# Kernel tuning notes

Hardware: AMD Instinct MI355X
Metric: run time of the kernel (lower is better)

## Reference

```python
import jax, jax.numpy as jnp
import numpy as np

B, N, T, F = 256, 64, 50, 2
E, H, R = 64, 128, 30


def setup_inputs() -> dict:
    key = jax.random.key(0)
    ks = jax.random.split(key, 16)
    rn = lambda k, shp, s=0.1: jax.random.normal(k, shp, jnp.float32) * s
    return {
        "src": jax.random.normal(ks[0], (B, N, T, F), jnp.float32),
        "trg": jax.random.normal(ks[1], (B, R, F), jnp.float32),
        # spatial encoder: residual Linear (no bias) + GCNConv weight/bias
        "W_res": rn(ks[2], (F, E)),
        "W_gcn": rn(ks[3], (F, E)),
        "b_gcn": jnp.zeros((E,), jnp.float32),
        # encoder LSTMCell (PyTorch gate order i,f,g,o); b = b_ih + b_hh fused
        "W_ih_e": rn(ks[4], (E, 4 * H)),
        "W_hh_e": rn(ks[5], (H, 4 * H)),
        "b_e": jnp.zeros((4 * H,), jnp.float32),
        # decoder: linear1 (2->E), LSTMCell (E->H), linear2 (H->2)
        "W1": rn(ks[6], (F, E)),
        "b1": jnp.zeros((E,), jnp.float32),
        "W_ih_d": rn(ks[7], (E, 4 * H)),
        "W_hh_d": rn(ks[8], (H, 4 * H)),
        "b_d": jnp.zeros((4 * H,), jnp.float32),
        "W2": rn(ks[9], (H, F)),
        "b2": jnp.zeros((F,), jnp.float32),
    }


def _lstm_step(h, c, xt, W_ih, W_hh, b):
    g = xt @ W_ih + h @ W_hh + b
    i, f, gg, o = jnp.split(g, 4, axis=-1)
    c = jax.nn.sigmoid(f) * c + jax.nn.sigmoid(i) * jnp.tanh(gg)
    h = jax.nn.sigmoid(o) * jnp.tanh(c)
    return h, c


def _forward(src, trg, W_res, W_gcn, b_gcn, W_ih_e, W_hh_e, b_e,
             W1, b1, W_ih_d, W_hh_d, b_d, W2, b2):
    # ---- EncoderSpatial: distance-weighted GCNConv over per-(sample,t) full graph ----
    x = jnp.swapaxes(src, 1, 2)                       # [B,T,N,F]
    diff = x[:, :, :, None, :] - x[:, :, None, :, :]  # [B,T,N,N,F]
    dist = jnp.linalg.norm(diff, axis=-1)             # [B,T,N,N]
    dist = jnp.where(dist == 0.0, 1e-6, dist)
    w = jnp.minimum(1.0 / dist, 1.0)                  # clipped inverse distance
    eye = jnp.eye(N, dtype=x.dtype)
    w = w * (1.0 - eye) + eye                         # remove self loops, GCN adds them with weight 1
    dinv = jnp.sum(w, axis=-1) ** -0.5                # [B,T,N]
    A = w * dinv[..., :, None] * dinv[..., None, :]   # sym-normalized adjacency
    gcn = jnp.einsum('btij,btjf->btif', A, x @ W_gcn) + b_gcn
    enc = jax.nn.relu(gcn + x @ W_res)                # [B,T,N,E]
    emb = enc[:, :, 0, :]                             # target-agent embeddings [B,T,E]
    inputs0 = x[:, :, 0, :]                           # target-agent positions  [B,T,F]

    # ---- LSTM encoder over T steps ----
    def enc_step(carry, xt):
        h, c = _lstm_step(carry[0], carry[1], xt, W_ih_e, W_hh_e, b_e)
        return (h, c), None
    h0 = jnp.zeros((B, H), src.dtype)
    (h, c), _ = jax.lax.scan(enc_step, (h0, h0), jnp.swapaxes(emb, 0, 1))

    def dec_step(carry, _):
        xin, h, c = carry
        ed = jax.nn.relu(xin @ W1 + b1)
        h, c = _lstm_step(h, c, ed, W_ih_d, W_hh_d, b_d)
        out = h @ W2 + b2
        return (out, h, c), out
    (_, _, _), outs = jax.lax.scan(dec_step, (inputs0[:, -1, :], h, c), None, length=R)
    return jnp.swapaxes(outs, 0, 1)                   # reg: [B,R,F]


def reference(src, trg, W_res, W_gcn, b_gcn, W_ih_e, W_hh_e, b_e,
              W1, b1, W_ih_d, W_hh_d, b_d, W2, b2):
    return _forward(src, trg, W_res, W_gcn, b_gcn, W_ih_e, W_hh_e, b_e,
                    W1, b1, W_ih_d, W_hh_d, b_d, W2, b2)
```

## Files before the change

### kernel.cpp

```cpp
#include <hip/hip_runtime.h>

#define Bn 256
#define Nn 64
#define Tn 50
#define Fn 2
#define En 64
#define Hn 128
#define Rn 30
#define G4 512

typedef _Float16 h2    __attribute__((ext_vector_type(2)));
typedef _Float16 f16x8 __attribute__((ext_vector_type(8)));
typedef float    f32x4 __attribute__((ext_vector_type(4)));

__device__ __forceinline__ float sigf(float x) {
    return __builtin_amdgcn_rcpf(1.0f + __expf(-x));
}
__device__ __forceinline__ float tanh_fast(float x) {
    return 1.0f - 2.0f * __builtin_amdgcn_rcpf(__expf(2.0f * x) + 1.0f);
}
__device__ __forceinline__ float dot2(h2 a, h2 b, float c) {
#if __has_builtin(__builtin_amdgcn_fdot2)
    return __builtin_amdgcn_fdot2(a, b, c, false);
#else
    return fmaf((float)a[0], (float)b[0], fmaf((float)a[1], (float)b[1], c));
#endif
}
__device__ __forceinline__ h2 pack2(float a, float b) {
    h2 r; r[0] = (_Float16)a; r[1] = (_Float16)b; return r;
}
__device__ __forceinline__ h2 bch2(float u)        { return __builtin_bit_cast(h2, u); }
__device__ __forceinline__ h2 bchu(unsigned int u) { return __builtin_bit_cast(h2, u); }

__device__ __forceinline__ void blockbar() {
    __builtin_amdgcn_sched_barrier(0);
    asm volatile("s_waitcnt lgkmcnt(0)" ::: "memory");
    __builtin_amdgcn_s_barrier();
    __builtin_amdgcn_sched_barrier(0);
}

__global__ __launch_bounds__(512) void k_pre(const float* __restrict__ src,
                                             const float* __restrict__ W_res,
                                             const float* __restrict__ W_gcn,
                                             const float* __restrict__ b_gcn,
                                             const float* __restrict__ W_ih_e,
                                             const float* __restrict__ b_e,
                                             _Float16* __restrict__ XI)
{
    const int tid  = threadIdx.x;
    const int lane = tid & 63;
    const int wv   = tid >> 6;
    const int task0 = blockIdx.x * 64;

    __shared__ __align__(16) _Float16 elds[64][64];
    __shared__ float2 xs[8][Nn];

    const float wg0 = W_gcn[lane], wg1 = W_gcn[En + lane];
    const float wr0 = W_res[lane], wr1 = W_res[En + lane];
    const float bg  = b_gcn[lane];

    for (int it = 0; it < 8; it++) {
        const int task = task0 + (wv << 3) + it;
        const int b = task / Tn;
        const int t = task - b * Tn;

        const float2 xv = *reinterpret_cast<const float2*>(
            src + (((size_t)b * Nn + lane) * Tn + t) * Fn);
        const float x0 = xv.x, x1 = xv.y;
        xs[wv][lane] = xv;

        float rowsum = 0.0f, w0 = 0.0f;
        #pragma unroll
        for (int k = 0; k < Nn; k++) {
            const float2 o = xs[wv][k];
            const float dx = x0 - o.x, dy = x1 - o.y;
            const float w = fminf(__builtin_amdgcn_rsqf(dx * dx + dy * dy), 1.0f);
            rowsum += w;
            if (k == 0) w0 = w;
        }
        const float dinv  = __builtin_amdgcn_rsqf(rowsum);
        const float dinv0 = __shfl(dinv, 0);
        const float a = w0 * dinv0 * dinv;

        float p0 = a * x0, p1 = a * x1;
        #pragma unroll
        for (int off = 32; off; off >>= 1) {
            p0 += __shfl_xor(p0, off);
            p1 += __shfl_xor(p1, off);
        }
        const float xa = __shfl(x0, 0);
        const float xb = __shfl(x1, 0);

        const float v = p0 * wg0 + p1 * wg1 + bg + xa * wr0 + xb * wr1;
        elds[(wv << 3) + it][lane] = (_Float16)fmaxf(v, 0.0f);
    }

    const int colp = (tid & 3) * 128 + (tid >> 2);
    h2 wih[32];
    #pragma unroll
    for (int q = 0; q < 32; q++)
        wih[q] = pack2(W_ih_e[(size_t)(2 * q) * G4 + colp],
                       W_ih_e[(size_t)(2 * q + 1) * G4 + colp]);
    const float be = b_e[colp];
    __syncthreads();

    for (int it = 0; it < 64; it++) {
        const float4* e4 = reinterpret_cast<const float4*>(&elds[it][0]);
        float acc = be;
        #pragma unroll
        for (int q = 0; q < 8; q++) {
            const float4 u = e4[q];
            acc = dot2(wih[4 * q + 0], bch2(u.x), acc);
            acc = dot2(wih[4 * q + 1], bch2(u.y), acc);
            acc = dot2(wih[4 * q + 2], bch2(u.z), acc);
            acc = dot2(wih[4 * q + 3], bch2(u.w), acc);
        }
        XI[(size_t)(task0 + it) * G4 + tid] = (_Float16)acc;
    }
}

__global__ __launch_bounds__(512) void k_seq(
    const _Float16* __restrict__ XI,
    const float* __restrict__ src,
    const float* __restrict__ W_hh_e,
    const float* __restrict__ W1,     const float* __restrict__ b1,
    const float* __restrict__ W_ih_d, const float* __restrict__ W_hh_d,
    const float* __restrict__ b_d,
    const float* __restrict__ W2,     const float* __restrict__ b2,
    float* __restrict__ out)
{
    const int tid  = threadIdx.x;
    const int lane = tid & 63;
    const int wv   = tid >> 6;
    const int l15  = lane & 15;
    const int lg   = lane >> 4;
    const int cc   = wv * 16 + l15;
    const int bq0  = blockIdx.x * 4;

    __shared__ __align__(16) _Float16 hbuf[2][576];
    __shared__ __align__(16) _Float16 edbuf[2][320];
    __shared__ __align__(16) _Float16 wi_frag[8 * 8 * 64 * 8];
    __shared__ __align__(16) float    redw[8][4][2];

    f16x8 bfr[4][4];
    #pragma unroll
    for (int g = 0; g < 4; g++)
        #pragma unroll
        for (int kt = 0; kt < 4; kt++) {
            f16x8 v;
            #pragma unroll
            for (int j = 0; j < 8; j++)
                v[j] = (_Float16)W_hh_e[(size_t)(kt * 32 + lg * 8 + j) * G4 + g * 128 + cc];
            bfr[g][kt] = v;
        }

    if (tid < 288) reinterpret_cast<float*>(&hbuf[0][0])[tid] = 0.0f;

    float cst = 0.0f;
    char* const hb0 = reinterpret_cast<char*>(&hbuf[0][0]);
    char* const hb1 = reinterpret_cast<char*>(&hbuf[1][0]);
    const _Float16* const XIrow = XI + (size_t)(bq0 + lg) * Tn * G4 + cc * 4;

    uint2 xi0, xi1;
    xi0 = *reinterpret_cast<const uint2*>(XIrow + 0 * G4);
    xi1 = *reinterpret_cast<const uint2*>(XIrow + 1 * G4);
    __syncthreads();

    for (int t = 0; t < Tn; t += 2) {
        uint2 nxt0, nxt1;
        const int t2 = (t + 2 < Tn) ? t + 2 : t;
        const int t3 = (t + 3 < Tn) ? t + 3 : t;
        nxt0 = *reinterpret_cast<const uint2*>(XIrow + (size_t)t2 * G4);
        nxt1 = *reinterpret_cast<const uint2*>(XIrow + (size_t)t3 * G4);

        #pragma unroll
        for (int half = 0; half < 2; half++) {
            char* const hr = half ? hb1 : hb0;
            char* const hw = half ? hb0 : hb1;
            const uint2 xiv = half ? xi1 : xi0;

            f16x8 af[4];
            #pragma unroll
            for (int kt = 0; kt < 4; kt++)
                af[kt] = *reinterpret_cast<const f16x8*>(
                    hr + (l15 & 3) * 288 + kt * 64 + lg * 16);

            f32x4 acc[4] = {};
            #pragma unroll
            for (int kt = 0; kt < 4; kt++)
                #pragma unroll
                for (int g = 0; g < 4; g++)
                    acc[g] = __builtin_amdgcn_mfma_f32_16x16x32_f16(af[kt], bfr[g][kt], acc[g], 0, 0, 0);

            float ga[4];
            #pragma unroll
            for (int g = 0; g < 4; g++) {
                const float s01 = (lg & 1) ? acc[g][1] : acc[g][0];
                const float s23 = (lg & 1) ? acc[g][3] : acc[g][2];
                ga[g] = (lg & 2) ? s23 : s01;
            }

            const h2 lo = bchu(xiv.x);
            const h2 hi = bchu(xiv.y);
            const float gi = ga[0] + (float)lo[0];
            const float gf = ga[1] + (float)lo[1];
            const float gg = ga[2] + (float)hi[0];
            const float go = ga[3] + (float)hi[1];
            cst = sigf(gf) * cst + sigf(gi) * tanh_fast(gg);
            const float hv = sigf(go) * tanh_fast(cst);

            *reinterpret_cast<_Float16*>(hw + lg * 288 + cc * 2) = (_Float16)hv;
            blockbar();
        }
        xi0 = nxt0; xi1 = nxt1;
    }

    #pragma unroll
    for (int g = 0; g < 4; g++)
        #pragma unroll
        for (int kt = 0; kt < 4; kt++) {
            f16x8 v;
            #pragma unroll
            for (int j = 0; j < 8; j++)
                v[j] = (_Float16)W_hh_d[(size_t)(kt * 32 + lg * 8 + j) * G4 + g * 128 + cc];
            bfr[g][kt] = v;
        }
    #pragma unroll
    for (int g = 0; g < 4; g++)
        #pragma unroll
        for (int kt2 = 0; kt2 < 2; kt2++) {
            f16x8 v;
            #pragma unroll
            for (int j = 0; j < 8; j++)
                v[j] = (_Float16)W_ih_d[(size_t)(kt2 * 32 + lg * 8 + j) * G4 + g * 128 + cc];
            *reinterpret_cast<f16x8*>(&wi_frag[((wv * 8 + g * 2 + kt2) * 64 + lane) * 8]) = v;
        }

    const float bd0 = b_d[cc], bd1 = b_d[128 + cc], bd2 = b_d[256 + cc], bd3 = b_d[384 + cc];
    const float w2a = W2[cc * 2], w2b = W2[cc * 2 + 1];
    const int   e   = (wv & 3) * 16 + l15;
    const float w1a = W1[e], w1b = W1[En + e], b1v = b1[e];
    const float b20 = b2[0], b21 = b2[1];

    char* const eb0 = reinterpret_cast<char*>(&edbuf[0][0]);
    char* const eb1 = reinterpret_cast<char*>(&edbuf[1][0]);

    if (wv < 4) {
        const float xin0 = src[((size_t)(bq0 + lg) * Nn * Tn + (Tn - 1)) * Fn + 0];
        const float xin1 = src[((size_t)(bq0 + lg) * Nn * Tn + (Tn - 1)) * Fn + 1];
        const float ed = fmaxf(xin0 * w1a + xin1 * w1b + b1v, 0.0f);
        *reinterpret_cast<_Float16*>(eb0 + lg * 160 + e * 2) = (_Float16)ed;
    }
    __syncthreads();

    for (int r = 0; r < Rn; r++) {
        const int cur = r & 1;
        char* const hr = cur ? hb1 : hb0;
        char* const hw = cur ? hb0 : hb1;
        char* const er = cur ? eb1 : eb0;
        char* const ew = cur ? eb0 : eb1;

        f16x8 af[4];
        #pragma unroll
        for (int kt = 0; kt < 4; kt++)
            af[kt] = *reinterpret_cast<const f16x8*>(
                hr + (l15 & 3) * 288 + kt * 64 + lg * 16);
        f16x8 ae[2];
        #pragma unroll
        for (int kt2 = 0; kt2 < 2; kt2++)
            ae[kt2] = *reinterpret_cast<const f16x8*>(
                er + (l15 & 3) * 160 + kt2 * 64 + lg * 16);

        f32x4 acc[4] = {};
        #pragma unroll
        for (int kt = 0; kt < 4; kt++)
            #pragma unroll
            for (int g = 0; g < 4; g++)
                acc[g] = __builtin_amdgcn_mfma_f32_16x16x32_f16(af[kt], bfr[g][kt], acc[g], 0, 0, 0);
        #pragma unroll
        for (int g = 0; g < 4; g++)
            #pragma unroll
            for (int kt2 = 0; kt2 < 2; kt2++) {
                const f16x8 bfe = *reinterpret_cast<const f16x8*>(
                    &wi_frag[((wv * 8 + g * 2 + kt2) * 64 + lane) * 8]);
                acc[g] = __builtin_amdgcn_mfma_f32_16x16x32_f16(ae[kt2], bfe, acc[g], 0, 0, 0);
            }

        float ga[4];
        #pragma unroll
        for (int g = 0; g < 4; g++) {
            const float s01 = (lg & 1) ? acc[g][1] : acc[g][0];
            const float s23 = (lg & 1) ? acc[g][3] : acc[g][2];
            ga[g] = (lg & 2) ? s23 : s01;
        }

        const float gi = ga[0] + bd0;
        const float gf = ga[1] + bd1;
        const float gg = ga[2] + bd2;
        const float go = ga[3] + bd3;
        cst = sigf(gf) * cst + sigf(gi) * tanh_fast(gg);
        const float hv = sigf(go) * tanh_fast(cst);
        *reinterpret_cast<_Float16*>(hw + lg * 288 + cc * 2) = (_Float16)hv;

        float p0 = hv * w2a, p1 = hv * w2b;
        #pragma unroll
        for (int off = 1; off < 16; off <<= 1) {
            p0 += __shfl_xor(p0, off);
            p1 += __shfl_xor(p1, off);
        }
        if (l15 == 0) { redw[wv][lg][0] = p0; redw[wv][lg][1] = p1; }
        blockbar();

        float o0 = b20, o1 = b21;
        #pragma unroll
        for (int w8 = 0; w8 < 8; w8++) {
            o0 += redw[w8][lg][0];
            o1 += redw[w8][lg][1];
        }
        if (wv == 4 && l15 < 2)
            out[(((size_t)(bq0 + lg)) * Rn + r) * Fn + l15] = l15 ? o1 : o0;
        if (wv < 4 && r + 1 < Rn) {
            const float ed = fmaxf(o0 * w1a + o1 * w1b + b1v, 0.0f);
            *reinterpret_cast<_Float16*>(ew + lg * 160 + e * 2) = (_Float16)ed;
        }
        blockbar();
    }
}

extern "C" void kernel_launch(void* const* d_in, const int* in_sizes, int n_in,
                              void* d_out, int out_size, void* d_ws, size_t ws_size,
                              hipStream_t stream)
{
    const float* src    = (const float*)d_in[0];
    const float* W_res  = (const float*)d_in[2];
    const float* W_gcn  = (const float*)d_in[3];
    const float* b_gcn  = (const float*)d_in[4];
    const float* W_ih_e = (const float*)d_in[5];
    const float* W_hh_e = (const float*)d_in[6];
    const float* b_e    = (const float*)d_in[7];
    const float* W1     = (const float*)d_in[8];
    const float* b1     = (const float*)d_in[9];
    const float* W_ih_d = (const float*)d_in[10];
    const float* W_hh_d = (const float*)d_in[11];
    const float* b_d    = (const float*)d_in[12];
    const float* W2     = (const float*)d_in[13];
    const float* b2     = (const float*)d_in[14];

    float* out = (float*)d_out;
    _Float16* XI = (_Float16*)d_ws;

    k_pre<<<(Bn * Tn) / 64, 512, 0, stream>>>(src, W_res, W_gcn, b_gcn, W_ih_e, b_e, XI);
    k_seq<<<Bn / 4, 512, 0, stream>>>(XI, src,
                                      W_hh_e,
                                      W1, b1,
                                      W_ih_d, W_hh_d, b_d,
                                      W2, b2, out);
}
```

Before: 102.6 us.

## Compute decoder embedding in registers, drop per-step barrier; shrink k_pre blocks

In the decoder loop each thread now builds the linear1+ReLU embedding MFMA fragment directly in registers, in packed fp16, from the reduced outputs o0/o1. This removes the edbuf shared buffer and the second block barrier per step. The reduction buffer is double-buffered by step parity so one barrier per step is enough. Separately, k_pre handles 16 tasks per block instead of 64, launching four times as many blocks for better occupancy, at the cost of reloading W_ih_e per block. The embedding math moves from fp32 to fp16, which may change accuracy slightly.

After: 104.8 us. +2.1%, slower.

```diff
diff --git a/kernel.cpp b/kernel.cpp
--- a/kernel.cpp
+++ b/kernel.cpp
@@ -50,17 +50,18 @@
     const int tid  = threadIdx.x;
     const int lane = tid & 63;
     const int wv   = tid >> 6;
-    const int task0 = blockIdx.x * 64;
-
-    __shared__ __align__(16) _Float16 elds[64][64];
+    const int task0 = blockIdx.x * 16;
+
+    __shared__ __align__(16) _Float16 elds[16][64];
     __shared__ float2 xs[8][Nn];
 
     const float wg0 = W_gcn[lane], wg1 = W_gcn[En + lane];
     const float wr0 = W_res[lane], wr1 = W_res[En + lane];
     const float bg  = b_gcn[lane];
 
-    for (int it = 0; it < 8; it++) {
-        const int task = task0 + (wv << 3) + it;
+    #pragma unroll
+    for (int it = 0; it < 2; it++) {
+        const int task = task0 + (wv << 1) + it;
         const int b = task / Tn;
         const int t = task - b * Tn;
 
@@ -92,7 +93,7 @@
         const float xb = __shfl(x1, 0);
 
         const float v = p0 * wg0 + p1 * wg1 + bg + xa * wr0 + xb * wr1;
-        elds[(wv << 3) + it][lane] = (_Float16)fmaxf(v, 0.0f);
+        elds[(wv << 1) + it][lane] = (_Float16)fmaxf(v, 0.0f);
     }
 
     const int colp = (tid & 3) * 128 + (tid >> 2);
@@ -104,7 +105,8 @@
     const float be = b_e[colp];
     __syncthreads();
 
-    for (int it = 0; it < 64; it++) {
+    #pragma unroll
+    for (int it = 0; it < 16; it++) {
         const float4* e4 = reinterpret_cast<const float4*>(&elds[it][0]);
         float acc = be;
         #pragma unroll
@@ -138,9 +140,8 @@
     const int bq0  = blockIdx.x * 4;
 
     __shared__ __align__(16) _Float16 hbuf[2][576];
-    __shared__ __align__(16) _Float16 edbuf[2][320];
     __shared__ __align__(16) _Float16 wi_frag[8 * 8 * 64 * 8];
-    __shared__ __align__(16) float    redw[8][4][2];
+    __shared__ __align__(16) float    redw[2][8][4][2];
 
     f16x8 bfr[4][4];
     #pragma unroll
@@ -238,38 +239,46 @@
 
     const float bd0 = b_d[cc], bd1 = b_d[128 + cc], bd2 = b_d[256 + cc], bd3 = b_d[384 + cc];
     const float w2a = W2[cc * 2], w2b = W2[cc * 2 + 1];
-    const int   e   = (wv & 3) * 16 + l15;
-    const float w1a = W1[e], w1b = W1[En + e], b1v = b1[e];
     const float b20 = b2[0], b21 = b2[1];
-
-    char* const eb0 = reinterpret_cast<char*>(&edbuf[0][0]);
-    char* const eb1 = reinterpret_cast<char*>(&edbuf[1][0]);
-
-    if (wv < 4) {
-        const float xin0 = src[((size_t)(bq0 + lg) * Nn * Tn + (Tn - 1)) * Fn + 0];
-        const float xin1 = src[((size_t)(bq0 + lg) * Nn * Tn + (Tn - 1)) * Fn + 1];
-        const float ed = fmaxf(xin0 * w1a + xin1 * w1b + b1v, 0.0f);
-        *reinterpret_cast<_Float16*>(eb0 + lg * 160 + e * 2) = (_Float16)ed;
-    }
+    const int   mb  = l15 & 3;
+
+    h2 w1ah[8], w1bh[8], b1h[8];
+    #pragma unroll
+    for (int q = 0; q < 8; q++) {
+        const int e0 = (q >> 2) * 32 + lg * 8 + (q & 3) * 2;
+        w1ah[q] = pack2(W1[e0],      W1[e0 + 1]);
+        w1bh[q] = pack2(W1[En + e0], W1[En + e0 + 1]);
+        b1h[q]  = pack2(b1[e0],      b1[e0 + 1]);
+    }
+
+    float o0 = src[((size_t)(bq0 + mb) * Nn * Tn + (Tn - 1)) * Fn + 0];
+    float o1 = src[((size_t)(bq0 + mb) * Nn * Tn + (Tn - 1)) * Fn + 1];
     __syncthreads();
 
     for (int r = 0; r < Rn; r++) {
         const int cur = r & 1;
         char* const hr = cur ? hb1 : hb0;
         char* const hw = cur ? hb0 : hb1;
-        char* const er = cur ? eb1 : eb0;
-        char* const ew = cur ? eb0 : eb1;
+
+        const h2 o0h = pack2(o0, o0);
+        const h2 o1h = pack2(o1, o1);
+        f16x8 ae[2];
+        #pragma unroll
+        for (int kt2 = 0; kt2 < 2; kt2++)
+            #pragma unroll
+            for (int p = 0; p < 4; p++) {
+                h2 v = w1ah[kt2 * 4 + p] * o0h + w1bh[kt2 * 4 + p] * o1h + b1h[kt2 * 4 + p];
+                v[0] = v[0] > (_Float16)0 ? v[0] : (_Float16)0;
+                v[1] = v[1] > (_Float16)0 ? v[1] : (_Float16)0;
+                ae[kt2][2 * p]     = v[0];
+                ae[kt2][2 * p + 1] = v[1];
+            }
 
         f16x8 af[4];
         #pragma unroll
         for (int kt = 0; kt < 4; kt++)
             af[kt] = *reinterpret_cast<const f16x8*>(
                 hr + (l15 & 3) * 288 + kt * 64 + lg * 16);
-        f16x8 ae[2];
-        #pragma unroll
-        for (int kt2 = 0; kt2 < 2; kt2++)
-            ae[kt2] = *reinterpret_cast<const f16x8*>(
-                er + (l15 & 3) * 160 + kt2 * 64 + lg * 16);
 
         f32x4 acc[4] = {};
         #pragma unroll
@@ -308,22 +317,24 @@
             p0 += __shfl_xor(p0, off);
             p1 += __shfl_xor(p1, off);
         }
-        if (l15 == 0) { redw[wv][lg][0] = p0; redw[wv][lg][1] = p1; }
+        if (l15 == 0) {
+            redw[cur][wv][lg][0] = p0;
+            redw[cur][wv][lg][1] = p1;
+        }
         blockbar();
 
-        float o0 = b20, o1 = b21;
+        o0 = b20; o1 = b21;
         #pragma unroll
         for (int w8 = 0; w8 < 8; w8++) {
-            o0 += redw[w8][lg][0];
-            o1 += redw[w8][lg][1];
-        }
-        if (wv == 4 && l15 < 2)
-            out[(((size_t)(bq0 + lg)) * Rn + r) * Fn + l15] = l15 ? o1 : o0;
-        if (wv < 4 && r + 1 < Rn) {
-            const float ed = fmaxf(o0 * w1a + o1 * w1b + b1v, 0.0f);
-            *reinterpret_cast<_Float16*>(ew + lg * 160 + e * 2) = (_Float16)ed;
-        }
-        blockbar();
+            const float2 rr = *reinterpret_cast<const float2*>(&redw[cur][w8][mb][0]);
+            o0 += rr.x; o1 += rr.y;
+        }
+        if (wv == 4 && l15 < 2) {
+            float oo = l15 ? b21 : b20;
+            #pragma unroll
+            for (int w8 = 0; w8 < 8; w8++) oo += redw[cur][w8][lg][l15];
+            out[(((size_t)(bq0 + lg)) * Rn + r) * Fn + l15] = oo;
+        }
     }
 }
 
@@ -349,7 +360,7 @@
     float* out = (float*)d_out;
     _Float16* XI = (_Float16*)d_ws;
 
-    k_pre<<<(Bn * Tn) / 64, 512, 0, stream>>>(src, W_res, W_gcn, b_gcn, W_ih_e, b_e, XI);
+    k_pre<<<(Bn * Tn) / 16, 512, 0, stream>>>(src, W_res, W_gcn, b_gcn, W_ih_e, b_e, XI);
     k_seq<<<Bn / 4, 512, 0, stream>>>(XI, src,
                                       W_hh_e,
                                       W1, b1,
```
